# Performance work log

Measured on AMD Instinct MI355X. Metric: run time of the kernel, lower is better.

The kernel has to match this reference:

```python
import jax, jax.numpy as jnp
import numpy as np

B, S, HID = 1, 4096, 2048
NH, NKV, HD = 8, 4, 256
SCALING = 256.0 ** -0.5
SOFT_CAP = 50.0
WINDOW = 4096
ROPE_THETA = 10000.0
NEG = jnp.finfo(jnp.float32).min


def _build_mask():
    q = np.arange(S)[:, None]
    k = np.arange(S)[None, :]
    causal = k <= q
    windowed = (q - k) < WINDOW
    allowed = causal & windowed
    m = np.where(allowed, 0.0, np.finfo(np.float32).min).astype(np.float32)
    return jnp.asarray(m)[None, None]  # [1,1,S,S]


def setup_inputs() -> dict:
    key = jax.random.key(0)
    ks = jax.random.split(key, 5)
    scale = 0.02
    return {
        "hidden_states": jax.random.normal(ks[0], (B, S, HID), jnp.float32),
        "attention_mask": _build_mask(),
        "position_ids": jnp.arange(S, dtype=jnp.int64)[None, :],
        "wq": jax.random.normal(ks[1], (HID, NH * HD), jnp.float32) * scale,
        "wk": jax.random.normal(ks[2], (HID, NKV * HD), jnp.float32) * scale,
        "wv": jax.random.normal(ks[3], (HID, NKV * HD), jnp.float32) * scale,
        "wo": jax.random.normal(ks[4], (NH * HD, HID), jnp.float32) * scale,
    }


def _rope(position_ids):
    inv_freq = 1.0 / (ROPE_THETA ** (jnp.arange(0, HD, 2, dtype=jnp.float32) / HD))
    freqs = position_ids.astype(jnp.float32)[:, :, None] * inv_freq[None, None, :]  # [B,S,HD/2]
    emb = jnp.concatenate([freqs, freqs], axis=-1)  # [B,S,HD]
    return jnp.cos(emb), jnp.sin(emb)


def _rotate_half(x):
    x1, x2 = x[..., : HD // 2], x[..., HD // 2 :]
    return jnp.concatenate([-x2, x1], axis=-1)


def _attn(hidden_states, attention_mask, position_ids, wq, wk, wv, wo):
    bsz, q_len, _ = hidden_states.shape
    q = (hidden_states @ wq).reshape(bsz, q_len, NH, HD).transpose(0, 2, 1, 3)    # [B,NH,S,HD]
    k = (hidden_states @ wk).reshape(bsz, q_len, NKV, HD).transpose(0, 2, 1, 3)   # [B,NKV,S,HD]
    v = (hidden_states @ wv).reshape(bsz, q_len, NKV, HD).transpose(0, 2, 1, 3)
    cos, sin = _rope(position_ids)
    cos, sin = cos[:, None], sin[:, None]  # [B,1,S,HD]
    q = q * cos + _rotate_half(q) * sin
    k = k * cos + _rotate_half(k) * sin
    n_rep = NH // NKV
    k = jnp.repeat(k, n_rep, axis=1)  # [B,NH,S,HD]
    v = jnp.repeat(v, n_rep, axis=1)
    scores = jnp.einsum("bhqd,bhkd->bhqk", q, k) * SCALING
    scores = jnp.tanh(scores / SOFT_CAP) * SOFT_CAP
    scores = scores + attention_mask
    probs = jax.nn.softmax(scores.astype(jnp.float32), axis=-1).astype(q.dtype)
    out = jnp.einsum("bhqk,bhkd->bhqd", probs, v)  # [B,NH,S,HD]
    out = out.transpose(0, 2, 1, 3).reshape(bsz, q_len, NH * HD)
    return out @ wo


def reference(hidden_states, attention_mask, position_ids, wq, wk, wv, wo):
    return _attn(hidden_states, attention_mask, position_ids, wq, wk, wv, wo)
```

## Files before the change

kernel.cpp:

```cpp
#include <hip/hip_runtime.h>


#define SEQ 4096
#define HIDDEN 2048
#define NHEADS 8
#define HDIM 256

typedef unsigned short u16;
typedef __attribute__((ext_vector_type(8))) __bf16 bf16x8;
typedef __attribute__((ext_vector_type(4))) float f32x4;
typedef __attribute__((ext_vector_type(16))) float f32x16;

static __device__ inline u16 f2bf(float f) {
  union { float f; unsigned u; } x; x.f = f;
  unsigned r = x.u + 0x7FFFu + ((x.u >> 16) & 1u);
  return (u16)(r >> 16);
}
static __device__ inline float bf2f(u16 u) {
  union { unsigned u; float f; } x; x.u = ((unsigned)u) << 16;
  return x.f;
}

typedef __attribute__((address_space(1))) const unsigned int* gp_t;
typedef __attribute__((address_space(3))) unsigned int* lp_t;
static __device__ inline void load_lds16(const u16* g, u16* l) {
  __builtin_amdgcn_global_load_lds((gp_t)g, (lp_t)l, 16, 0, 0);
}


__global__ void convert_hs_kernel(const float* __restrict__ src, u16* __restrict__ dst) {
  int i = blockIdx.x * 256 + threadIdx.x;
  float4 v = ((const float4*)src)[i];
  ushort4 o;
  o.x = f2bf(v.x); o.y = f2bf(v.y); o.z = f2bf(v.z); o.w = f2bf(v.w);
  ((ushort4*)dst)[i] = o;
}

__global__ void transpose_w_kernel(const float* __restrict__ src, u16* __restrict__ dst,
                                   int K, int N) {
  __shared__ u16 tile[64][65];
  int n0 = blockIdx.x * 64, k0 = blockIdx.y * 64;
  int tid = threadIdx.x;
  for (int i = 0; i < 16; i++) {
    int idx = i * 256 + tid; int r = idx >> 6, c = idx & 63;
    tile[r][c] = f2bf(src[(size_t)(k0 + r) * N + n0 + c]);
  }
  __syncthreads();
  for (int i = 0; i < 16; i++) {
    int idx = i * 256 + tid; int r = idx >> 6, c = idx & 63;
    dst[(size_t)(n0 + r) * K + k0 + c] = tile[c][r];
  }
}

__global__ void rope_kernel(u16* qkv) {
  int idx = blockIdx.x * 256 + threadIdx.x;
  int s = idx / (12 * 128);
  int rem = idx - s * (12 * 128);
  int head = rem >> 7;
  int i = rem & 127;
  float inv = __expf(-(float)i * 0.0719557841560639f);
  float ang = (float)s * inv;
  float sn, cs;
  sincosf(ang, &sn, &cs);
  size_t base = (size_t)s * 4096 + head * 256 + i;
  float a = bf2f(qkv[base]);
  float b = bf2f(qkv[base + 128]);
  qkv[base]       = f2bf(a * cs - b * sn);
  qkv[base + 128] = f2bf(b * cs + a * sn);
}

__global__ void transpose_v_kernel(const u16* __restrict__ qkv, u16* __restrict__ vT) {
  __shared__ u16 tile[64][65];
  int d0 = blockIdx.x * 64, s0 = blockIdx.y * 64;
  int tid = threadIdx.x;
  for (int i = 0; i < 16; i++) {
    int idx = i * 256 + tid; int r = idx >> 6, c = idx & 63;
    tile[r][c] = qkv[(size_t)(s0 + r) * 4096 + 3072 + d0 + c];
  }
  __syncthreads();
  for (int i = 0; i < 16; i++) {
    int idx = i * 256 + tid; int r = idx >> 6, c = idx & 63;
    vT[(size_t)(d0 + r) * 4096 + s0 + c] = tile[c][r];
  }
}


template <bool OUT_F32>
__global__ __launch_bounds__(256, 2) void gemm_bf16_kernel(
    const u16* __restrict__ A, const u16* __restrict__ Bt, void* __restrict__ Cout,
    int M, int N, int K) {
  __shared__ __attribute__((aligned(16))) u16 As[128 * 64];
  __shared__ __attribute__((aligned(16))) u16 Bs[128 * 64];
  int tid = threadIdx.x;
  int wave = tid >> 6, lane = tid & 63;
  int lm = lane & 15, qd = lane >> 4;
  int m0 = blockIdx.y * 128, n0 = blockIdx.x * 128;
  int wm = (wave >> 1) * 64, wn = (wave & 1) * 64;

  f32x4 acc[4][4];
#pragma unroll
  for (int a = 0; a < 4; a++)
#pragma unroll
    for (int b = 0; b < 4; b++) acc[a][b] = (f32x4){0.f, 0.f, 0.f, 0.f};

  int srow = lane >> 3;
  int scol = (lane & 7) * 8;

  for (int kt = 0; kt < K; kt += 64) {
    __syncthreads();
#pragma unroll
    for (int t = 0; t < 4; t++) {
      int j = wave * 4 + t;
      int row = j * 8 + srow;
      load_lds16(A  + (size_t)(m0 + row) * K + kt + scol, As + j * 512);
      load_lds16(Bt + (size_t)(n0 + row) * K + kt + scol, Bs + j * 512);
    }
    __syncthreads();
#pragma unroll
    for (int kk = 0; kk < 2; kk++) {
      bf16x8 af[4], bfr[4];
#pragma unroll
      for (int mi = 0; mi < 4; mi++)
        af[mi] = *(const bf16x8*)&As[(wm + mi * 16 + lm) * 64 + kk * 32 + qd * 8];
#pragma unroll
      for (int ni = 0; ni < 4; ni++)
        bfr[ni] = *(const bf16x8*)&Bs[(wn + ni * 16 + lm) * 64 + kk * 32 + qd * 8];
#pragma unroll
      for (int mi = 0; mi < 4; mi++)
#pragma unroll
        for (int ni = 0; ni < 4; ni++)
          acc[mi][ni] = __builtin_amdgcn_mfma_f32_16x16x32_bf16(af[mi], bfr[ni],
                                                               acc[mi][ni], 0, 0, 0);
    }
  }
#pragma unroll
  for (int mi = 0; mi < 4; mi++) {
    int row = m0 + wm + mi * 16 + qd * 4;
#pragma unroll
    for (int ni = 0; ni < 4; ni++) {
      int col = n0 + wn + ni * 16 + lm;
#pragma unroll
      for (int r = 0; r < 4; r++) {
        float v = acc[mi][ni][r];
        if (OUT_F32) ((float*)Cout)[(size_t)(row + r) * N + col] = v;
        else         ((u16*)Cout)[(size_t)(row + r) * N + col] = f2bf(v);
      }
    }
  }
}


__global__ __launch_bounds__(256, 2) void flash_kernel(
    const u16* __restrict__ qkv, const u16* __restrict__ vT,
    u16* __restrict__ attn) {
  __shared__ __attribute__((aligned(16))) u16 Ks[64 * 256];
  __shared__ __attribute__((aligned(16))) u16 Vs[256 * 64];
  __shared__ __attribute__((aligned(16))) u16 Pl[64 * 64];

  int tid = threadIdx.x;
  int w = tid >> 6, lane = tid & 63;
  int l31 = lane & 31, hi = lane >> 5;
  int qhalf = w >> 1, kh = w & 1, dhalf = w & 1;

  int b = blockIdx.x;
  int r = b & 255;
  int h = r & 7;
  int pi = r >> 3;
  int qt = (b >> 8) ? (63 - pi) : pi;
  int kvh = h >> 1;
  int T = qt + 1;
  int qs = qt * 64 + qhalf * 32;

  int vlc = (lane & 7) ^ ((lane >> 3) & 7);
  int vro = lane >> 3;

  const u16* Kg  = qkv + 2048 + (size_t)kvh * 256;
  const u16* Vg0 = vT + (size_t)(kvh * 256) * 4096;

  bf16x8 ones;
#pragma unroll
  for (int e = 0; e < 8; e++) ones[e] = (__bf16)1.0f;

  {
    const u16* Qg = qkv + (size_t)(qt * 64) * 4096 + h * 256;
#pragma unroll
    for (int s = 0; s < 8; s++) {
      int kr = (w * 8 + s) * 2 + hi;
      int klc = l31 ^ (kr & 31);
      load_lds16(Qg + (size_t)kr * 4096 + klc * 8, &Ks[(w * 8 + s) * 512]);
    }
  }
  __syncthreads();

  bf16x8 aq[16];
#pragma unroll
  for (int kc = 0; kc < 16; kc++)
    aq[kc] = *(const bf16x8*)&Ks[(qhalf * 32 + l31) * 256 +
                                 (((kc * 2 + hi) ^ l31) << 3)];
  __syncthreads();

  f32x16 ao[4];
#pragma unroll
  for (int g = 0; g < 4; g++) ao[g] = (f32x16)(0.f);
  f32x16 al = (f32x16)(0.f);

  for (int t = 0; t < T; t++) {
    {
      const u16* Kt = Kg + (size_t)(t * 64) * 4096;
      const u16* Vt = Vg0 + t * 64;
#pragma unroll
      for (int s = 0; s < 8; s++) {
        int kr = (w * 8 + s) * 2 + hi;
        int klc = l31 ^ (kr & 31);
        load_lds16(Kt + (size_t)kr * 4096 + klc * 8, &Ks[(w * 8 + s) * 512]);
        int vr = (w * 8 + s) * 8 + vro;
        load_lds16(Vt + (size_t)vr * 4096 + vlc * 8, &Vs[(w * 8 + s) * 512]);
      }
    }
    __syncthreads();

    f32x16 se = (f32x16)(0.f);
    f32x16 so = (f32x16)(0.f);
#pragma unroll
    for (int kc = 0; kc < 8; kc++) {
      bf16x8 bk0 = *(const bf16x8*)&Ks[(kh * 32 + l31) * 256 +
                                       ((((2 * kc) * 2 + hi) ^ l31) << 3)];
      se = __builtin_amdgcn_mfma_f32_32x32x16_bf16(aq[2 * kc], bk0, se, 0, 0, 0);
      bf16x8 bk1 = *(const bf16x8*)&Ks[(kh * 32 + l31) * 256 +
                                       ((((2 * kc + 1) * 2 + hi) ^ l31) << 3)];
      so = __builtin_amdgcn_mfma_f32_32x32x16_bf16(aq[2 * kc + 1], bk1, so, 0, 0, 0);
    }
    f32x16 sacc = se + so;

    bool diag = (t == T - 1);
#pragma unroll
    for (int reg = 0; reg < 16; reg++) {
      int qa = 4 * hi + 8 * (reg >> 2) + (reg & 3);
      int q64 = qhalf * 32 + qa;
      int key64 = kh * 32 + l31;
      float x = sacc[reg] * 0.00125f;
      float x2 = x * x;
      float th = x * (1.f + x2 * (-0.33333333f + x2 * 0.13333333f));
      float p = exp2f(72.134752f * (th - 1.f));
      if (diag && key64 > q64) p = 0.f;
      Pl[q64 * 64 + (((key64 >> 3) ^ (q64 & 7)) << 3) + (key64 & 7)] = f2bf(p);
    }
    __syncthreads();

    bf16x8 ap[4];
#pragma unroll
    for (int kc = 0; kc < 4; kc++)
      ap[kc] = *(const bf16x8*)&Pl[(qhalf * 32 + l31) * 64 +
                                   (((kc * 2 + hi) ^ (l31 & 7)) << 3)];
#pragma unroll
    for (int g = 0; g < 4; g++) {
      int dd = dhalf * 128 + g * 32 + l31;
#pragma unroll
      for (int kc = 0; kc < 4; kc++) {
        bf16x8 bv = *(const bf16x8*)&Vs[dd * 64 +
                                        (((kc * 2 + hi) ^ (l31 & 7)) << 3)];
        ao[g] = __builtin_amdgcn_mfma_f32_32x32x16_bf16(ap[kc], bv, ao[g], 0, 0, 0);
      }
    }
#pragma unroll
    for (int kc = 0; kc < 4; kc++)
      al = __builtin_amdgcn_mfma_f32_32x32x16_bf16(ap[kc], ones, al, 0, 0, 0);

    __syncthreads();
  }

  float inv_l[16];
#pragma unroll
  for (int reg = 0; reg < 16; reg++) inv_l[reg] = 1.f / al[reg];
#pragma unroll
  for (int g = 0; g < 4; g++) {
    int col = h * 256 + dhalf * 128 + g * 32 + l31;
#pragma unroll
    for (int reg = 0; reg < 16; reg++) {
      int row = qs + 4 * hi + 8 * (reg >> 2) + (reg & 3);
      attn[(size_t)row * 2048 + col] = f2bf(ao[g][reg] * inv_l[reg]);
    }
  }
}


extern "C" void kernel_launch(void* const* d_in, const int* in_sizes, int n_in,
                              void* d_out, int out_size, void* d_ws, size_t ws_size,
                              hipStream_t stream) {
  const float* hs = (const float*)d_in[0];
  const float* wq = (const float*)d_in[3];
  const float* wk = (const float*)d_in[4];
  const float* wv = (const float*)d_in[5];
  const float* wo = (const float*)d_in[6];
  float* out = (float*)d_out;

  char* ws = (char*)d_ws;
  u16* hsb    = (u16*)(ws);
  u16* wqkvT  = (u16*)(ws + 16777216);
  u16* woT    = (u16*)(ws + 33554432);
  u16* qkv    = (u16*)(ws + 41943040);
  u16* vT     = (u16*)(ws + 75497472);
  u16* attn   = (u16*)(ws + 83886080);

  convert_hs_kernel<<<8192, 256, 0, stream>>>(hs, hsb);
  transpose_w_kernel<<<dim3(32, 32), 256, 0, stream>>>(wq, wqkvT, HIDDEN, 2048);
  transpose_w_kernel<<<dim3(16, 32), 256, 0, stream>>>(wk, wqkvT + (size_t)2048 * HIDDEN, HIDDEN, 1024);
  transpose_w_kernel<<<dim3(16, 32), 256, 0, stream>>>(wv, wqkvT + (size_t)3072 * HIDDEN, HIDDEN, 1024);
  transpose_w_kernel<<<dim3(32, 32), 256, 0, stream>>>(wo, woT, HIDDEN, 2048);

  gemm_bf16_kernel<false><<<dim3(32, 32), 256, 0, stream>>>(hsb, wqkvT, qkv, 4096, 4096, 2048);
  rope_kernel<<<24576, 256, 0, stream>>>(qkv);
  transpose_v_kernel<<<dim3(16, 64), 256, 0, stream>>>(qkv, vT);

  flash_kernel<<<512, 256, 0, stream>>>(qkv, vT, attn);
  gemm_bf16_kernel<true><<<dim3(16, 32), 256, 0, stream>>>(attn, woT, out, 4096, 2048, 2048);
}
```

Before: 506.9 us.

## Split long causal query tiles across two blocks and combine partial results

The flash kernel now gives each pair of blocks balanced work. Each A block handles a short query tile, then the first part of the KV range for a long query tile. Each B block handles the remaining KV range for that long tile. The unnormalized partial outputs and row sums go to fp32 scratch buffers that reuse dead workspace regions, and a new combine kernel adds them, normalizes and writes bf16. This is meant to remove the tail where some blocks process up to 64 KV tiles while others process one. The cost is an extra Q load per segment, fp32 partial-output traffic and one extra kernel launch.

```diff
diff --git a/kernel.cpp b/kernel.cpp
--- a/kernel.cpp
+++ b/kernel.cpp
@@ -152,7 +152,8 @@
 
 __global__ __launch_bounds__(256, 2) void flash_kernel(
     const u16* __restrict__ qkv, const u16* __restrict__ vT,
-    u16* __restrict__ attn) {
+    u16* __restrict__ attn, float* __restrict__ PA, float* __restrict__ PB,
+    float* __restrict__ lbuf ) {
   __shared__ __attribute__((aligned(16))) u16 Ks[64 * 256];
   __shared__ __attribute__((aligned(16))) u16 Vs[256 * 64];
   __shared__ __attribute__((aligned(16))) u16 Pl[64 * 64];
@@ -166,10 +167,9 @@
   int r = b & 255;
   int h = r & 7;
   int pi = r >> 3;
-  int qt = (b >> 8) ? (63 - pi) : pi;
   int kvh = h >> 1;
-  int T = qt + 1;
-  int qs = qt * 64 + qhalf * 32;
+  int isA = (b < 256);
+  int nseg = isA ? 2 : 1;
 
   int vlc = (lane & 7) ^ ((lane >> 3) & 7);
   int vro = lane >> 3;
@@ -181,105 +181,161 @@
 #pragma unroll
   for (int e = 0; e < 8; e++) ones[e] = (__bf16)1.0f;
 
-  {
-    const u16* Qg = qkv + (size_t)(qt * 64) * 4096 + h * 256;
-#pragma unroll
-    for (int s = 0; s < 8; s++) {
-      int kr = (w * 8 + s) * 2 + hi;
-      int klc = l31 ^ (kr & 31);
-      load_lds16(Qg + (size_t)kr * 4096 + klc * 8, &Ks[(w * 8 + s) * 512]);
-    }
-  }
-  __syncthreads();
-
-  bf16x8 aq[16];
-#pragma unroll
-  for (int kc = 0; kc < 16; kc++)
-    aq[kc] = *(const bf16x8*)&Ks[(qhalf * 32 + l31) * 256 +
-                                 (((kc * 2 + hi) ^ l31) << 3)];
-  __syncthreads();
-
-  f32x16 ao[4];
-#pragma unroll
-  for (int g = 0; g < 4; g++) ao[g] = (f32x16)(0.f);
-  f32x16 al = (f32x16)(0.f);
-
-  for (int t = 0; t < T; t++) {
+  for (int si = 0; si < nseg; si++) {
+    int qt, k0, k1, mode;
+    if (isA && si == 0) { qt = pi;      k0 = 0;       k1 = pi + 1;  mode = 0; }
+    else if (isA)       { qt = 63 - pi; k0 = 0;       k1 = 31 - pi; mode = 1; }
+    else                { qt = 63 - pi; k0 = 31 - pi; k1 = 64 - pi; mode = 2; }
+
     {
-      const u16* Kt = Kg + (size_t)(t * 64) * 4096;
-      const u16* Vt = Vg0 + t * 64;
+      const u16* Qg = qkv + (size_t)(qt * 64) * 4096 + h * 256;
 #pragma unroll
       for (int s = 0; s < 8; s++) {
         int kr = (w * 8 + s) * 2 + hi;
         int klc = l31 ^ (kr & 31);
-        load_lds16(Kt + (size_t)kr * 4096 + klc * 8, &Ks[(w * 8 + s) * 512]);
-        int vr = (w * 8 + s) * 8 + vro;
-        load_lds16(Vt + (size_t)vr * 4096 + vlc * 8, &Vs[(w * 8 + s) * 512]);
+        load_lds16(Qg + (size_t)kr * 4096 + klc * 8, &Ks[(w * 8 + s) * 512]);
       }
     }
     __syncthreads();
 
-    f32x16 se = (f32x16)(0.f);
-    f32x16 so = (f32x16)(0.f);
-#pragma unroll
-    for (int kc = 0; kc < 8; kc++) {
-      bf16x8 bk0 = *(const bf16x8*)&Ks[(kh * 32 + l31) * 256 +
-                                       ((((2 * kc) * 2 + hi) ^ l31) << 3)];
-      se = __builtin_amdgcn_mfma_f32_32x32x16_bf16(aq[2 * kc], bk0, se, 0, 0, 0);
-      bf16x8 bk1 = *(const bf16x8*)&Ks[(kh * 32 + l31) * 256 +
-                                       ((((2 * kc + 1) * 2 + hi) ^ l31) << 3)];
-      so = __builtin_amdgcn_mfma_f32_32x32x16_bf16(aq[2 * kc + 1], bk1, so, 0, 0, 0);
-    }
-    f32x16 sacc = se + so;
-
-    bool diag = (t == T - 1);
-#pragma unroll
-    for (int reg = 0; reg < 16; reg++) {
-      int qa = 4 * hi + 8 * (reg >> 2) + (reg & 3);
-      int q64 = qhalf * 32 + qa;
-      int key64 = kh * 32 + l31;
-      float x = sacc[reg] * 0.00125f;
-      float x2 = x * x;
-      float th = x * (1.f + x2 * (-0.33333333f + x2 * 0.13333333f));
-      float p = exp2f(72.134752f * (th - 1.f));
-      if (diag && key64 > q64) p = 0.f;
-      Pl[q64 * 64 + (((key64 >> 3) ^ (q64 & 7)) << 3) + (key64 & 7)] = f2bf(p);
-    }
+    bf16x8 aq[16];
+#pragma unroll
+    for (int kc = 0; kc < 16; kc++)
+      aq[kc] = *(const bf16x8*)&Ks[(qhalf * 32 + l31) * 256 +
+                                   (((kc * 2 + hi) ^ l31) << 3)];
     __syncthreads();
 
-    bf16x8 ap[4];
-#pragma unroll
-    for (int kc = 0; kc < 4; kc++)
-      ap[kc] = *(const bf16x8*)&Pl[(qhalf * 32 + l31) * 64 +
-                                   (((kc * 2 + hi) ^ (l31 & 7)) << 3)];
-#pragma unroll
-    for (int g = 0; g < 4; g++) {
-      int dd = dhalf * 128 + g * 32 + l31;
-#pragma unroll
-      for (int kc = 0; kc < 4; kc++) {
-        bf16x8 bv = *(const bf16x8*)&Vs[dd * 64 +
-                                        (((kc * 2 + hi) ^ (l31 & 7)) << 3)];
-        ao[g] = __builtin_amdgcn_mfma_f32_32x32x16_bf16(ap[kc], bv, ao[g], 0, 0, 0);
-      }
-    }
-#pragma unroll
-    for (int kc = 0; kc < 4; kc++)
-      al = __builtin_amdgcn_mfma_f32_32x32x16_bf16(ap[kc], ones, al, 0, 0, 0);
-
-    __syncthreads();
-  }
-
-  float inv_l[16];
-#pragma unroll
-  for (int reg = 0; reg < 16; reg++) inv_l[reg] = 1.f / al[reg];
-#pragma unroll
-  for (int g = 0; g < 4; g++) {
-    int col = h * 256 + dhalf * 128 + g * 32 + l31;
-#pragma unroll
-    for (int reg = 0; reg < 16; reg++) {
-      int row = qs + 4 * hi + 8 * (reg >> 2) + (reg & 3);
-      attn[(size_t)row * 2048 + col] = f2bf(ao[g][reg] * inv_l[reg]);
-    }
+    f32x16 ao[4];
+#pragma unroll
+    for (int g = 0; g < 4; g++) ao[g] = (f32x16)(0.f);
+    f32x16 al = (f32x16)(0.f);
+
+    for (int t = k0; t < k1; t++) {
+      {
+        const u16* Kt = Kg + (size_t)(t * 64) * 4096;
+        const u16* Vt = Vg0 + t * 64;
+#pragma unroll
+        for (int s = 0; s < 8; s++) {
+          int kr = (w * 8 + s) * 2 + hi;
+          int klc = l31 ^ (kr & 31);
+          load_lds16(Kt + (size_t)kr * 4096 + klc * 8, &Ks[(w * 8 + s) * 512]);
+          int vr = (w * 8 + s) * 8 + vro;
+          load_lds16(Vt + (size_t)vr * 4096 + vlc * 8, &Vs[(w * 8 + s) * 512]);
+        }
+      }
+      __syncthreads();
+
+      f32x16 se = (f32x16)(0.f);
+      f32x16 so = (f32x16)(0.f);
+#pragma unroll
+      for (int kc = 0; kc < 8; kc++) {
+        bf16x8 bk0 = *(const bf16x8*)&Ks[(kh * 32 + l31) * 256 +
+                                         ((((2 * kc) * 2 + hi) ^ l31) << 3)];
+        se = __builtin_amdgcn_mfma_f32_32x32x16_bf16(aq[2 * kc], bk0, se, 0, 0, 0);
+        bf16x8 bk1 = *(const bf16x8*)&Ks[(kh * 32 + l31) * 256 +
+                                         ((((2 * kc + 1) * 2 + hi) ^ l31) << 3)];
+        so = __builtin_amdgcn_mfma_f32_32x32x16_bf16(aq[2 * kc + 1], bk1, so, 0, 0, 0);
+      }
+      f32x16 sacc = se + so;
+
+      bool diag = (t == qt);
+#pragma unroll
+      for (int reg = 0; reg < 16; reg++) {
+        int qa = 4 * hi + 8 * (reg >> 2) + (reg & 3);
+        int q64 = qhalf * 32 + qa;
+        int key64 = kh * 32 + l31;
+        float x = sacc[reg] * 0.00125f;
+        float x2 = x * x;
+        float th = x * (1.f + x2 * (-0.33333333f + x2 * 0.13333333f));
+        float p = exp2f(72.134752f * (th - 1.f));
+        if (diag && key64 > q64) p = 0.f;
+        Pl[q64 * 64 + (((key64 >> 3) ^ (q64 & 7)) << 3) + (key64 & 7)] = f2bf(p);
+      }
+      __syncthreads();
+
+      bf16x8 ap[4];
+#pragma unroll
+      for (int kc = 0; kc < 4; kc++)
+        ap[kc] = *(const bf16x8*)&Pl[(qhalf * 32 + l31) * 64 +
+                                     (((kc * 2 + hi) ^ (l31 & 7)) << 3)];
+#pragma unroll
+      for (int g = 0; g < 4; g++) {
+        int dd = dhalf * 128 + g * 32 + l31;
+#pragma unroll
+        for (int kc = 0; kc < 4; kc++) {
+          bf16x8 bv = *(const bf16x8*)&Vs[dd * 64 +
+                                          (((kc * 2 + hi) ^ (l31 & 7)) << 3)];
+          ao[g] = __builtin_amdgcn_mfma_f32_32x32x16_bf16(ap[kc], bv, ao[g], 0, 0, 0);
+        }
+      }
+#pragma unroll
+      for (int kc = 0; kc < 4; kc++)
+        al = __builtin_amdgcn_mfma_f32_32x32x16_bf16(ap[kc], ones, al, 0, 0, 0);
+
+      __syncthreads();
+    }
+
+    if (mode == 0) {
+      float inv_l[16];
+#pragma unroll
+      for (int reg = 0; reg < 16; reg++) inv_l[reg] = 1.f / al[reg];
+      int qs = qt * 64 + qhalf * 32;
+#pragma unroll
+      for (int g = 0; g < 4; g++) {
+        int col = h * 256 + dhalf * 128 + g * 32 + l31;
+#pragma unroll
+        for (int reg = 0; reg < 16; reg++) {
+          int row = qs + 4 * hi + 8 * (reg >> 2) + (reg & 3);
+          attn[(size_t)row * 2048 + col] = f2bf(ao[g][reg] * inv_l[reg]);
+        }
+      }
+    } else {
+      float* Pbuf = (mode == 1) ? PA : PB;
+#pragma unroll
+      for (int g = 0; g < 4; g++) {
+        int col = dhalf * 128 + g * 32 + l31;
+#pragma unroll
+        for (int reg = 0; reg < 16; reg++) {
+          int row = qhalf * 32 + 4 * hi + 8 * (reg >> 2) + (reg & 3);
+          Pbuf[((size_t)r * 64 + row) * 256 + col] = ao[g][reg];
+        }
+      }
+      if (dhalf == 0 && l31 == 0) {
+        size_t lbase = (size_t)(r * 16 + (mode - 1)) * 2048 + 1536;
+#pragma unroll
+        for (int reg = 0; reg < 16; reg++) {
+          int row = qhalf * 32 + 4 * hi + 8 * (reg >> 2) + (reg & 3);
+          lbuf[lbase + row] = al[reg];
+        }
+      }
+    }
+  }
+}
+
+__global__ __launch_bounds__(256) void combine_kernel(
+    const float* __restrict__ PA, const float* __restrict__ PB,
+    const float* __restrict__ lbuf, u16* __restrict__ attn) {
+  int p = blockIdx.x;
+  int h = p & 7, pi = p >> 3;
+  int qt2 = 63 - pi;
+  int tid = threadIdx.x;
+  int row = tid >> 2;
+  int c0 = (tid & 3) * 64;
+  float la = lbuf[(size_t)(p * 16) * 2048 + 1536 + row];
+  float lb = lbuf[(size_t)(p * 16 + 1) * 2048 + 1536 + row];
+  float inv = 1.f / (la + lb);
+  size_t src = ((size_t)p * 64 + row) * 256 + c0;
+  size_t dst = (size_t)(qt2 * 64 + row) * 2048 + h * 256 + c0;
+#pragma unroll
+  for (int c = 0; c < 64; c += 4) {
+    float4 a = *(const float4*)&PA[src + c];
+    float4 bb = *(const float4*)&PB[src + c];
+    ushort4 o;
+    o.x = f2bf((a.x + bb.x) * inv);
+    o.y = f2bf((a.y + bb.y) * inv);
+    o.z = f2bf((a.z + bb.z) * inv);
+    o.w = f2bf((a.w + bb.w) * inv);
+    *(ushort4*)&attn[dst + c] = o;
   }
 }
 
@@ -301,6 +357,9 @@
   u16* qkv    = (u16*)(ws + 41943040);
   u16* vT     = (u16*)(ws + 75497472);
   u16* attn   = (u16*)(ws + 83886080);
+  float* PA   = (float*)(ws);
+  float* PB   = (float*)(ws + 16777216);
+  float* lbuf = (float*)(ws + 41943040);
 
   convert_hs_kernel<<<8192, 256, 0, stream>>>(hs, hsb);
   transpose_w_kernel<<<dim3(32, 32), 256, 0, stream>>>(wq, wqkvT, HIDDEN, 2048);
@@ -312,6 +371,7 @@
   rope_kernel<<<24576, 256, 0, stream>>>(qkv);
   transpose_v_kernel<<<dim3(16, 64), 256, 0, stream>>>(qkv, vT);
 
-  flash_kernel<<<512, 256, 0, stream>>>(qkv, vT, attn);
+  flash_kernel<<<512, 256, 0, stream>>>(qkv, vT, attn, PA, PB, lbuf);
+  combine_kernel<<<256, 256, 0, stream>>>(PA, PB, lbuf, attn);
   gemm_bf16_kernel<true><<<dim3(16, 32), 256, 0, stream>>>(attn, woT, out, 4096, 2048, 2048);
 }
```

New measurement: 482.6 us. 4.8% less time.
